# Optimization experiments

Measured on AMD Instinct MI355X. Metric: run time of the kernel, lower is better.

## Reference

```python
import jax, jax.numpy as jnp
import numpy as np

D_MODEL = 1024
N_HEADS = 16
D_K = D_MODEL // N_HEADS
THETA = 10000.0
NEG_INF = -1e30


def _rope_tables(token_positions, d_k, theta=THETA):
    # freqs[t, i] = t / theta**(2i/d_k), i in [0, d_k/2)
    exponent = jnp.arange(0, d_k, 2, dtype=jnp.float32)  # [d_k/2]
    inv_freq = 1.0 / theta ** (exponent / d_k)
    freqs = token_positions.astype(jnp.float32)[:, None] * inv_freq[None, :]  # [s, d_k/2]
    return jnp.cos(freqs), jnp.sin(freqs)


def _apply_rope(x, cos, sin):
    # x: [..., s, d_k]; interleaved pair rotation (pairs are (x[2i], x[2i+1]))
    x1 = x[..., 0::2]
    x2 = x[..., 1::2]
    r1 = x1 * cos - x2 * sin
    r2 = x1 * sin + x2 * cos
    return jnp.stack([r1, r2], axis=-1).reshape(x.shape)


def setup_inputs() -> dict:
    key = jax.random.key(0)
    ks = jax.random.split(key, 5)
    b, s = 2, 2048
    scale = np.sqrt(2.0 / (D_MODEL + D_MODEL))
    return {
        "x": jax.random.normal(ks[0], (b, s, D_MODEL), dtype=jnp.float32),
        "Wq": jax.random.normal(ks[1], (D_MODEL, D_MODEL), dtype=jnp.float32) * scale,
        "Wk": jax.random.normal(ks[2], (D_MODEL, D_MODEL), dtype=jnp.float32) * scale,
        "Wv": jax.random.normal(ks[3], (D_MODEL, D_MODEL), dtype=jnp.float32) * scale,
        "Wo": jax.random.normal(ks[4], (D_MODEL, D_MODEL), dtype=jnp.float32) * scale,
        "token_positions": jnp.arange(s, dtype=jnp.int64 if jax.config.jax_enable_x64 else jnp.int32),
    }


def reference(x, Wq, Wk, Wv, Wo, token_positions):
    b, s, _ = x.shape
    # QKV projections: weight stored [in, out]
    q = jnp.einsum('bsi,io->bso', x, Wq)
    k = jnp.einsum('bsi,io->bso', x, Wk)
    v = jnp.einsum('bsi,io->bso', x, Wv)
    # split heads: [b, h, s, d_k]
    q = q.reshape(b, s, N_HEADS, D_K).transpose(0, 2, 1, 3)
    k = k.reshape(b, s, N_HEADS, D_K).transpose(0, 2, 1, 3)
    v = v.reshape(b, s, N_HEADS, D_K).transpose(0, 2, 1, 3)
    # RoPE
    cos, sin = _rope_tables(token_positions, D_K)
    q = _apply_rope(q, cos, sin)
    k = _apply_rope(k, cos, sin)
    # causal attention with full materialized scores (faithful to source)
    scores = jnp.einsum('bhid,bhjd->bhij', q, k) / jnp.sqrt(jnp.float32(D_K))
    mask = jnp.tril(jnp.ones((s, s), dtype=bool))
    scores = jnp.where(mask, scores, NEG_INF)
    probs = jax.nn.softmax(scores, axis=-1)
    out = jnp.einsum('bhij,bhjd->bhid', probs, v)
    out = out.transpose(0, 2, 1, 3).reshape(b, s, D_MODEL)
    return jnp.einsum('bsi,io->bso', out, Wo)
```

## Files before the change

kernel.cpp:

```cpp
#include <hip/hip_runtime.h>
#include <hip/hip_bf16.h>
#include <cmath>

#define S_LEN 2048
#define DMODEL 1024
#define NHEADS 16
#define DK 64
#define BATCH 2
#define MTOT (BATCH * S_LEN)

using short8 = __attribute__((ext_vector_type(8))) short;
using floatx4 = __attribute__((ext_vector_type(4))) float;

__device__ __forceinline__ unsigned short f2b(float f) {
    union { float f; unsigned u; } v; v.f = f;
    unsigned r = v.u + 0x7fff + ((v.u >> 16) & 1);
    return (unsigned short)(r >> 16);
}

__device__ __forceinline__ unsigned pack2(float a, float b) {
    float2 t; t.x = a; t.y = b;
    __hip_bfloat162 h = __float22bfloat162_rn(t);
    union { __hip_bfloat162 h; unsigned u; } v; v.h = h;
    return v.u;
}

__device__ __forceinline__ void gload16(const void* g, void* l) {
    __builtin_amdgcn_global_load_lds(
        (const __attribute__((address_space(1))) unsigned int*)g,
        (__attribute__((address_space(3))) unsigned int*)l, 16, 0, 0);
}

#define FENCE() asm volatile("" ::: "memory")

__global__ __launch_bounds__(256) void prep_k(
    const float* __restrict__ x, unsigned short* __restrict__ xb,
    const int* __restrict__ tokpos, float* __restrict__ ct, float* __restrict__ st,
    const float* W0, const float* W1, const float* W2, const float* W3,
    unsigned short* T0, unsigned short* T1, unsigned short* T2, unsigned short* T3) {
    __shared__ float t[64][65];
    const int b = blockIdx.x;
    if (b < 2048) {
        int i = (b * 256 + threadIdx.x) * 8;
        float4 a = *(const float4*)(x + i);
        float4 bb = *(const float4*)(x + i + 4);
        short8 o;
        o[0] = f2b(a.x); o[1] = f2b(a.y); o[2] = f2b(a.z); o[3] = f2b(a.w);
        o[4] = f2b(bb.x); o[5] = f2b(bb.y); o[6] = f2b(bb.z); o[7] = f2b(bb.w);
        *(short8*)(xb + i) = o;
    } else if (b < 2304) {
        int idx = (b - 2048) * 256 + threadIdx.x;
        int si = idx >> 5;
        int ip = idx & 31;
        float pos = (float)tokpos[si];
        float inv_freq = powf(10000.0f, -(float)(2 * ip) / 64.0f);
        float ang = pos * inv_freq;
        ct[idx] = cosf(ang);
        st[idx] = sinf(ang);
    } else {
        int id = b - 2304;
        int z = id >> 8;
        int bx = id & 15, by = (id >> 4) & 15;
        const float* W = z == 0 ? W0 : z == 1 ? W1 : z == 2 ? W2 : W3;
        unsigned short* T = z == 0 ? T0 : z == 1 ? T1 : z == 2 ? T2 : T3;
        const bool perm = (z < 2);
        int n0 = bx * 64, k0 = by * 64;
        int rr = threadIdx.x >> 6, cc = threadIdx.x & 63;
#pragma unroll
        for (int r = 0; r < 16; r++) {
            int row = r * 4 + rr;
            t[row][cc] = W[(size_t)(k0 + row) * DMODEL + n0 + cc];
        }
        __syncthreads();
#pragma unroll
        for (int r = 0; r < 16; r++) {
            int row = r * 4 + rr;
            int drow = perm ? (((row & 1) ? 32 : 0) + (row >> 1)) : row;
            T[(size_t)(n0 + drow) * DMODEL + k0 + cc] = f2b(t[cc][row]);
        }
    }
}

__global__ __launch_bounds__(256) void add_k(float* __restrict__ out,
                                             const float* __restrict__ p) {
    int i = (blockIdx.x * 256 + threadIdx.x) * 8;
    float4 a = *(const float4*)(out + i);
    float4 b = *(const float4*)(p + i);
    float4 c = *(const float4*)(out + i + 4);
    float4 d = *(const float4*)(p + i + 4);
    a.x += b.x; a.y += b.y; a.z += b.z; a.w += b.w;
    c.x += d.x; c.y += d.y; c.z += d.z; c.w += d.w;
    *(float4*)(out + i) = a;
    *(float4*)(out + i + 4) = c;
}

__global__ __launch_bounds__(256) void vtrans_k(const unsigned short* __restrict__ V,
                                                unsigned short* __restrict__ Vt) {
    __shared__ unsigned short t[64][72];
    const int tid = threadIdx.x;
    const int s0 = blockIdx.x * 64, d0 = blockIdx.y * 64;
    const int bb = s0 >> 11;
#pragma unroll
    for (int it = 0; it < 4; it++) {
        int e = (it * 256 + tid) * 4;
        int r = e >> 6, c = e & 63;
        *(ushort4*)&t[r][c] = *(const ushort4*)(V + (size_t)(s0 + r) * DMODEL + d0 + c);
    }
    __syncthreads();
#pragma unroll
    for (int it = 0; it < 4; it++) {
        int e = (it * 256 + tid) * 4;
        int r = e >> 6, c = e & 63;
        ushort4 v;
        v.x = t[c + 0][r]; v.y = t[c + 1][r];
        v.z = t[c + 2][r]; v.w = t[c + 3][r];
        *(ushort4*)(Vt + (size_t)(bb * 1024 + d0 + r) * S_LEN + (s0 & (S_LEN - 1)) + c) = v;
    }
}

__global__ __launch_bounds__(512, 2) void mm_k(
    const unsigned short* __restrict__ A,
    const unsigned short* __restrict__ Bt0, const unsigned short* __restrict__ Bt1,
    const unsigned short* __restrict__ Bt2,
    void* C0, void* C1, void* C2,
    const float* __restrict__ ct, const float* __restrict__ st, int kind) {
    __shared__ __align__(16) unsigned short blob[10 * 8192];

    const int z = blockIdx.z;
    const unsigned short* Bt = (kind == 1) ? Bt0 : (z == 0 ? Bt0 : z == 1 ? Bt1 : Bt2);
    void* C = (kind == 1) ? (z == 0 ? C0 : C1) : (z == 0 ? C0 : z == 1 ? C1 : C2);
    const int mode = (kind == 1) ? 0 : (z == 2 ? 3 : 1);
    const int t0 = (kind == 1) ? z * 8 : 0;
    const int NT = (kind == 1) ? 8 : 16;
    const float qscale = (z == 0 && kind == 0) ? 0.18033688011112042f : 1.0f;

    const int tid = threadIdx.x;
    const int w = tid >> 6, lane = tid & 63;
    const int l15 = lane & 15, quad = lane >> 4;
    const int wr = w >> 2, wc = w & 3;
    const int m0 = blockIdx.x * 256, n0 = blockIdx.y * 256;

    const int rbase = (w >> 1) * 16 + l15;
    const int cbase = (w & 1) * 32 + quad * 8;

    floatx4 acc[8][4];
#pragma unroll
    for (int i = 0; i < 8; i++)
#pragma unroll
        for (int j = 0; j < 4; j++) acc[i][j] = (floatx4){0.f, 0.f, 0.f, 0.f};

    auto stage_half = [&](int h) {
        const int ts = t0 + (h >> 2), part = h & 3;
        const int slot = h % 10;
        const unsigned short* src =
            (part < 2 ? A + (((size_t)(m0 + part * 128 + rbase)) << 10)
                      : Bt + (((size_t)(n0 + (part - 2) * 128 + rbase)) << 10))
            + (size_t)ts * 64 + cbase;
        char* d = (char*)blob + slot * 16384 + w * 1024;
        gload16(src, d);
        gload16(src + (64 << 10), d + 8192);
    };

#pragma unroll
    for (int h = 0; h < 6; ++h) stage_half(h);
    asm volatile("s_waitcnt vmcnt(4)" ::: "memory");
    FENCE(); __builtin_amdgcn_s_barrier(); FENCE();

    short8 af[4][2];
    for (int t = 0; t < NT; ++t) {
        const int sb = (4 * t) % 10;
        int sA = sb + wr;            if (sA >= 10) sA -= 10;
        int sB = sb + 2 + (wc >> 1); if (sB >= 10) sB -= 10;
        const char* LA = (const char*)blob + sA * 16384;
        const char* LB = (const char*)blob + sB * 16384;
#pragma unroll
        for (int q = 0; q < 4; ++q) {
            const int rh = q >> 1, ch = q & 1;
            if (ch == 0) {
#pragma unroll
                for (int ii = 0; ii < 4; ++ii)
#pragma unroll
                    for (int kh = 0; kh < 2; ++kh)
                        af[ii][kh] = *(const short8*)(LA + ((rh * 4 + ii) * 2 + kh) * 1024 + lane * 16);
            }
            short8 bf[2][2];
#pragma unroll
            for (int jj = 0; jj < 2; ++jj)
#pragma unroll
                for (int kh = 0; kh < 2; ++kh)
                    bf[jj][kh] = *(const short8*)(LB + (((wc & 1) * 4 + ch * 2 + jj) * 2 + kh) * 1024 + lane * 16);
            const int h = 4 * t + q + 6;
            if (h < 4 * NT) stage_half(h);
            if (q == 3) {
                if (t == NT - 2) asm volatile("s_waitcnt vmcnt(0)" ::: "memory");
                else             asm volatile("s_waitcnt vmcnt(4)" ::: "memory");
            }
            FENCE(); __builtin_amdgcn_s_barrier(); FENCE();
            __builtin_amdgcn_s_setprio(1);
#pragma unroll
            for (int ii = 0; ii < 4; ++ii)
#pragma unroll
                for (int jj = 0; jj < 2; ++jj) {
                    floatx4 a0 = acc[rh * 4 + ii][ch * 2 + jj];
                    a0 = __builtin_amdgcn_mfma_f32_16x16x32_bf16(af[ii][0], bf[jj][0], a0, 0, 0, 0);
                    a0 = __builtin_amdgcn_mfma_f32_16x16x32_bf16(af[ii][1], bf[jj][1], a0, 0, 0, 0);
                    acc[rh * 4 + ii][ch * 2 + jj] = a0;
                }
            __builtin_amdgcn_s_setprio(0);
            FENCE(); __builtin_amdgcn_s_barrier(); FENCE();
        }
    }

#pragma unroll
    for (int i = 0; i < 8; i++) {
        const int rowb = m0 + wr * 128 + i * 16 + quad * 4;
        if (mode == 0) {
            float* Cf = (float*)C;
#pragma unroll
            for (int j = 0; j < 4; j++) {
                int colb = n0 + wc * 64 + j * 16 + l15;
#pragma unroll
                for (int r = 0; r < 4; r++)
                    Cf[(size_t)(rowb + r) * DMODEL + colb] = acc[i][j][r];
            }
        } else if (mode == 1) {
            unsigned short* Cb = (unsigned short*)C;
#pragma unroll
            for (int jh = 0; jh < 2; jh++) {
                int ip = jh * 16 + l15;
                int cole = n0 + wc * 64 + jh * 16 + l15;
#pragma unroll
                for (int r = 0; r < 4; r++) {
                    int row = rowb + r;
                    int si = row & (S_LEN - 1);
                    float c = ct[si * 32 + ip] * qscale;
                    float s = st[si * 32 + ip] * qscale;
                    float e = acc[i][jh][r];
                    float od = acc[i][jh + 2][r];
                    Cb[(size_t)row * DMODEL + cole] = f2b(e * c - od * s);
                    Cb[(size_t)row * DMODEL + cole + 32] = f2b(e * s + od * c);
                }
            }
        } else {
            unsigned short* Cb = (unsigned short*)C;
#pragma unroll
            for (int j = 0; j < 4; j++) {
                int colb = n0 + wc * 64 + j * 16 + l15;
#pragma unroll
                for (int r = 0; r < 4; r++)
                    Cb[(size_t)(rowb + r) * DMODEL + colb] = f2b(acc[i][j][r]);
            }
        }
    }
}

__global__ __launch_bounds__(512) void attn_k(const unsigned short* __restrict__ Q,
                                              const unsigned short* __restrict__ K,
                                              const unsigned short* __restrict__ Vt,
                                              unsigned short* __restrict__ O) {
    __shared__ __align__(16) unsigned short Kblob[2][4096];
    __shared__ __align__(16) unsigned short Vblob[2][4096];
    __shared__ __align__(16) unsigned short Ps[8][16 * 72];

    const int tid = threadIdx.x;
    const int w = tid >> 6, lane = tid & 63;
    const int l15 = lane & 15, quad = lane >> 4;
    const int idx = blockIdx.x;
    const int qt = 15 - (idx >> 5);
    const int bh = idx & 31;
    const int bb = bh >> 4, h = bh & 15;
    const int qbase = qt * 128 + w * 16;
    const int qrow = qbase + l15;

    const size_t qoff = (size_t)(bb * S_LEN + qbase + l15) * DMODEL + h * DK;
    short8 aq0 = *(const short8*)(Q + qoff + quad * 8);
    short8 aq1 = *(const short8*)(Q + qoff + 32 + quad * 8);

    floatx4 o[4];
#pragma unroll
    for (int f = 0; f < 4; f++) o[f] = (floatx4){0.f, 0.f, 0.f, 0.f};
    float mv = -1e30f, lv = 0.f;

    const unsigned short* Kb = K + (size_t)(bb * S_LEN) * DMODEL + h * DK;
    const unsigned short* Vb = Vt + (size_t)(bb * 1024 + h * DK) * S_LEN;
    unsigned short* ps = &Ps[w][0];

    auto stage = [&](int b, int kb) {
#pragma unroll
        for (int it = 0; it < 2; it++) {
            int g = it * 8 + w;
            if (g < 8) {
                const unsigned short* gp =
                    Kb + (size_t)(kb + (g >> 1) * 16 + l15) * DMODEL + (g & 1) * 32 + quad * 8;
                gload16(gp, (char*)&Kblob[b][0] + g * 1024);
            } else {
                int gv = g - 8;
                const unsigned short* gp =
                    Vb + (size_t)((gv >> 1) * 16 + l15) * S_LEN + kb + (gv & 1) * 32 + quad * 8;
                gload16(gp, (char*)&Vblob[b][0] + gv * 1024);
            }
        }
    };

    const int nkt = 2 * qt + 2;
    stage(0, 0);
    for (int kt = 0; kt < nkt; kt++) {
        const int b = kt & 1;
        const int kb = kt * 64;
        __syncthreads();
        if (kt + 1 < nkt) stage(b ^ 1, (kt + 1) * 64);

        if (kb <= qbase + 15) {
            const unsigned short* kbb = &Kblob[b][0];
            floatx4 c[4];
            __builtin_amdgcn_s_setprio(1);
#pragma unroll
            for (int g = 0; g < 4; g++) {
                short8 kf0 = *(const short8*)(kbb + (g * 2 + 0) * 512 + lane * 8);
                short8 kf1 = *(const short8*)(kbb + (g * 2 + 1) * 512 + lane * 8);
                floatx4 t = {0.f, 0.f, 0.f, 0.f};
                t = __builtin_amdgcn_mfma_f32_16x16x32_bf16(kf0, aq0, t, 0, 0, 0);
                c[g] = __builtin_amdgcn_mfma_f32_16x16x32_bf16(kf1, aq1, t, 0, 0, 0);
            }
            __builtin_amdgcn_s_setprio(0);

            float sv[16];
            if (kb + 63 <= qbase) {
#pragma unroll
                for (int g = 0; g < 4; g++)
#pragma unroll
                    for (int r = 0; r < 4; r++) sv[g * 4 + r] = c[g][r];
            } else {
#pragma unroll
                for (int g = 0; g < 4; g++)
#pragma unroll
                    for (int r = 0; r < 4; r++) {
                        int key = kb + g * 16 + quad * 4 + r;
                        sv[g * 4 + r] = (key <= qrow) ? c[g][r] : -1e30f;
                    }
            }
            float t0 = fmaxf(fmaxf(sv[0], sv[1]), sv[2]);
            float t1 = fmaxf(fmaxf(sv[3], sv[4]), sv[5]);
            float t2 = fmaxf(fmaxf(sv[6], sv[7]), sv[8]);
            float t3 = fmaxf(fmaxf(sv[9], sv[10]), sv[11]);
            float t4 = fmaxf(fmaxf(sv[12], sv[13]), sv[14]);
            float mx = fmaxf(fmaxf(fmaxf(t0, t1), fmaxf(t2, t3)), fmaxf(t4, sv[15]));
            mx = fmaxf(mx, __shfl_xor(mx, 16));
            mx = fmaxf(mx, __shfl_xor(mx, 32));

            if (!__all(mx <= mv)) {
                float mnew = fmaxf(mv, mx);
                float alpha = exp2f(mv - mnew);
                mv = mnew;
                lv *= alpha;
#pragma unroll
                for (int f = 0; f < 4; f++) {
                    o[f][0] *= alpha; o[f][1] *= alpha;
                    o[f][2] *= alpha; o[f][3] *= alpha;
                }
            }
            float p[16], psum = 0.f;
#pragma unroll
            for (int i = 0; i < 16; i++) {
                p[i] = exp2f(sv[i] - mv);
                psum += p[i];
            }
            lv += psum;

#pragma unroll
            for (int g = 0; g < 4; g++) {
                uint2 pk;
                pk.x = pack2(p[g * 4 + 0], p[g * 4 + 1]);
                pk.y = pack2(p[g * 4 + 2], p[g * 4 + 3]);
                *(uint2*)(ps + l15 * 72 + g * 16 + quad * 4) = pk;
            }
            short8 pf0 = *(const short8*)(ps + l15 * 72 + quad * 8);
            short8 pf1 = *(const short8*)(ps + l15 * 72 + 32 + quad * 8);
            const unsigned short* vbb = &Vblob[b][0];
            __builtin_amdgcn_s_setprio(1);
#pragma unroll
            for (int f = 0; f < 4; f++) {
                short8 vf0 = *(const short8*)(vbb + (f * 2 + 0) * 512 + lane * 8);
                short8 vf1 = *(const short8*)(vbb + (f * 2 + 1) * 512 + lane * 8);
                o[f] = __builtin_amdgcn_mfma_f32_16x16x32_bf16(vf0, pf0, o[f], 0, 0, 0);
                o[f] = __builtin_amdgcn_mfma_f32_16x16x32_bf16(vf1, pf1, o[f], 0, 0, 0);
            }
            __builtin_amdgcn_s_setprio(0);
        }
    }

    lv += __shfl_xor(lv, 16);
    lv += __shfl_xor(lv, 32);
    float inv = 1.0f / lv;
    __syncthreads();
#pragma unroll
    for (int f = 0; f < 4; f++) {
        uint2 pk;
        pk.x = pack2(o[f][0] * inv, o[f][1] * inv);
        pk.y = pack2(o[f][2] * inv, o[f][3] * inv);
        *(uint2*)(ps + l15 * 72 + f * 16 + quad * 4) = pk;
    }
    short8 r0 = *(const short8*)(ps + l15 * 72 + quad * 8);
    short8 r1 = *(const short8*)(ps + l15 * 72 + 32 + quad * 8);
    size_t obase = (size_t)(bb * S_LEN + qbase + l15) * DMODEL + h * DK;
    *(short8*)(O + obase + quad * 8) = r0;
    *(short8*)(O + obase + 32 + quad * 8) = r1;
}

extern "C" void kernel_launch(void* const* d_in, const int* in_sizes, int n_in,
                              void* d_out, int out_size, void* d_ws,
                              size_t ws_size, hipStream_t stream) {
    const float* x = (const float*)d_in[0];
    const float* Wq = (const float*)d_in[1];
    const float* Wk = (const float*)d_in[2];
    const float* Wv = (const float*)d_in[3];
    const float* Wo = (const float*)d_in[4];
    const int* tokpos = (const int*)d_in[5];
    float* out = (float*)d_out;

    const size_t MD = (size_t)MTOT * DMODEL;
    const size_t WD = (size_t)DMODEL * DMODEL;
    unsigned short* xb = (unsigned short*)d_ws;
    unsigned short* Wqt = xb + MD;
    unsigned short* Wkt = Wqt + WD;
    unsigned short* Wvt = Wkt + WD;
    unsigned short* Wot = Wvt + WD;
    unsigned short* Q = Wot + WD;
    unsigned short* K = Q + MD;
    unsigned short* V = K + MD;
    unsigned short* Vt = V + MD;
    float* ct = (float*)(Vt + MD);
    float* st = ct + S_LEN * 32;
    unsigned short* O = V;
    float* P1 = (float*)Q;

    prep_k<<<dim3(3328), dim3(256), 0, stream>>>(x, xb, tokpos, ct, st,
                                                 Wq, Wk, Wv, Wo, Wqt, Wkt, Wvt, Wot);

    mm_k<<<dim3(16, 4, 3), dim3(512), 0, stream>>>(xb, Wqt, Wkt, Wvt,
                                                   (void*)Q, (void*)K, (void*)V, ct, st, 0);
    vtrans_k<<<dim3(64, 16), dim3(256), 0, stream>>>(V, Vt);
    attn_k<<<dim3(512), dim3(512), 0, stream>>>(Q, K, Vt, O);
    mm_k<<<dim3(16, 4, 2), dim3(512), 0, stream>>>(O, Wot, Wot, Wot,
                                                   (void*)out, (void*)P1, (void*)P1, ct, st, 1);
    add_k<<<dim3(2048), dim3(256), 0, stream>>>(out, P1);
}
```

Baseline: 211.2 us.

## Process two 16-row query groups per wave in attention, halving block width

The attention kernel now runs 4 waves per block instead of 8, and each wave handles 32 query rows as two 16-row groups. Each K and V fragment read from shared memory feeds MFMAs for both groups, which halves LDS reads per unit of compute, and each wave carries two independent MFMA chains. The cost is roughly double the accumulator and softmax register state per wave and fewer waves per block, which may cut occupancy and the latency hiding that came from having more waves. The causal skip is now decided per 32-row band, so some MFMA work on fully masked tiles is added.

```diff
diff --git a/kernel.cpp b/kernel.cpp
--- a/kernel.cpp
+++ b/kernel.cpp
@@ -254,13 +254,13 @@
     }
 }
 
-__global__ __launch_bounds__(512) void attn_k(const unsigned short* __restrict__ Q,
+__global__ __launch_bounds__(256) void attn_k(const unsigned short* __restrict__ Q,
                                               const unsigned short* __restrict__ K,
                                               const unsigned short* __restrict__ Vt,
                                               unsigned short* __restrict__ O) {
     __shared__ __align__(16) unsigned short Kblob[2][4096];
     __shared__ __align__(16) unsigned short Vblob[2][4096];
-    __shared__ __align__(16) unsigned short Ps[8][16 * 72];
+    __shared__ __align__(16) unsigned short Ps[4][32 * 72];
 
     const int tid = threadIdx.x;
     const int w = tid >> 6, lane = tid & 63;
@@ -269,17 +269,22 @@
     const int qt = 15 - (idx >> 5);
     const int bh = idx & 31;
     const int bb = bh >> 4, h = bh & 15;
-    const int qbase = qt * 128 + w * 16;
-    const int qrow = qbase + l15;
-
-    const size_t qoff = (size_t)(bb * S_LEN + qbase + l15) * DMODEL + h * DK;
-    short8 aq0 = *(const short8*)(Q + qoff + quad * 8);
-    short8 aq1 = *(const short8*)(Q + qoff + 32 + quad * 8);
-
-    floatx4 o[4];
-#pragma unroll
-    for (int f = 0; f < 4; f++) o[f] = (floatx4){0.f, 0.f, 0.f, 0.f};
-    float mv = -1e30f, lv = 0.f;
+    const int qb_w = qt * 128 + w * 32;
+
+    short8 aq[2][2];
+#pragma unroll
+    for (int qg = 0; qg < 2; qg++) {
+        const size_t qoff = (size_t)(bb * S_LEN + qb_w + qg * 16 + l15) * DMODEL + h * DK;
+        aq[qg][0] = *(const short8*)(Q + qoff + quad * 8);
+        aq[qg][1] = *(const short8*)(Q + qoff + 32 + quad * 8);
+    }
+
+    floatx4 o[2][4];
+#pragma unroll
+    for (int qg = 0; qg < 2; qg++)
+#pragma unroll
+        for (int f = 0; f < 4; f++) o[qg][f] = (floatx4){0.f, 0.f, 0.f, 0.f};
+    float mv[2] = {-1e30f, -1e30f}, lv[2] = {0.f, 0.f};
 
     const unsigned short* Kb = K + (size_t)(bb * S_LEN) * DMODEL + h * DK;
     const unsigned short* Vb = Vt + (size_t)(bb * 1024 + h * DK) * S_LEN;
@@ -287,8 +292,8 @@
 
     auto stage = [&](int b, int kb) {
 #pragma unroll
-        for (int it = 0; it < 2; it++) {
-            int g = it * 8 + w;
+        for (int it = 0; it < 4; it++) {
+            int g = it * 4 + w;
             if (g < 8) {
                 const unsigned short* gp =
                     Kb + (size_t)(kb + (g >> 1) * 16 + l15) * DMODEL + (g & 1) * 32 + quad * 8;
@@ -310,101 +315,119 @@
         __syncthreads();
         if (kt + 1 < nkt) stage(b ^ 1, (kt + 1) * 64);
 
-        if (kb <= qbase + 15) {
+        if (kb <= qb_w + 31) {
             const unsigned short* kbb = &Kblob[b][0];
-            floatx4 c[4];
+            floatx4 c[4][2];
             __builtin_amdgcn_s_setprio(1);
 #pragma unroll
             for (int g = 0; g < 4; g++) {
                 short8 kf0 = *(const short8*)(kbb + (g * 2 + 0) * 512 + lane * 8);
                 short8 kf1 = *(const short8*)(kbb + (g * 2 + 1) * 512 + lane * 8);
-                floatx4 t = {0.f, 0.f, 0.f, 0.f};
-                t = __builtin_amdgcn_mfma_f32_16x16x32_bf16(kf0, aq0, t, 0, 0, 0);
-                c[g] = __builtin_amdgcn_mfma_f32_16x16x32_bf16(kf1, aq1, t, 0, 0, 0);
+#pragma unroll
+                for (int qg = 0; qg < 2; qg++) {
+                    floatx4 t = {0.f, 0.f, 0.f, 0.f};
+                    t = __builtin_amdgcn_mfma_f32_16x16x32_bf16(kf0, aq[qg][0], t, 0, 0, 0);
+                    c[g][qg] = __builtin_amdgcn_mfma_f32_16x16x32_bf16(kf1, aq[qg][1], t, 0, 0, 0);
+                }
             }
             __builtin_amdgcn_s_setprio(0);
 
-            float sv[16];
-            if (kb + 63 <= qbase) {
-#pragma unroll
-                for (int g = 0; g < 4; g++)
-#pragma unroll
-                    for (int r = 0; r < 4; r++) sv[g * 4 + r] = c[g][r];
-            } else {
-#pragma unroll
-                for (int g = 0; g < 4; g++)
-#pragma unroll
-                    for (int r = 0; r < 4; r++) {
-                        int key = kb + g * 16 + quad * 4 + r;
-                        sv[g * 4 + r] = (key <= qrow) ? c[g][r] : -1e30f;
+#pragma unroll
+            for (int qg = 0; qg < 2; qg++) {
+                const int qbg = qb_w + qg * 16;
+                const int qrow = qbg + l15;
+                float sv[16];
+                if (kb + 63 <= qbg) {
+#pragma unroll
+                    for (int g = 0; g < 4; g++)
+#pragma unroll
+                        for (int r = 0; r < 4; r++) sv[g * 4 + r] = c[g][qg][r];
+                } else {
+#pragma unroll
+                    for (int g = 0; g < 4; g++)
+#pragma unroll
+                        for (int r = 0; r < 4; r++) {
+                            int key = kb + g * 16 + quad * 4 + r;
+                            sv[g * 4 + r] = (key <= qrow) ? c[g][qg][r] : -1e30f;
+                        }
+                }
+                float t0 = fmaxf(fmaxf(sv[0], sv[1]), sv[2]);
+                float t1 = fmaxf(fmaxf(sv[3], sv[4]), sv[5]);
+                float t2 = fmaxf(fmaxf(sv[6], sv[7]), sv[8]);
+                float t3 = fmaxf(fmaxf(sv[9], sv[10]), sv[11]);
+                float t4 = fmaxf(fmaxf(sv[12], sv[13]), sv[14]);
+                float mx = fmaxf(fmaxf(fmaxf(t0, t1), fmaxf(t2, t3)), fmaxf(t4, sv[15]));
+                mx = fmaxf(mx, __shfl_xor(mx, 16));
+                mx = fmaxf(mx, __shfl_xor(mx, 32));
+
+                if (!__all(mx <= mv[qg])) {
+                    float mnew = fmaxf(mv[qg], mx);
+                    float alpha = exp2f(mv[qg] - mnew);
+                    mv[qg] = mnew;
+                    lv[qg] *= alpha;
+#pragma unroll
+                    for (int f = 0; f < 4; f++) {
+                        o[qg][f][0] *= alpha; o[qg][f][1] *= alpha;
+                        o[qg][f][2] *= alpha; o[qg][f][3] *= alpha;
                     }
-            }
-            float t0 = fmaxf(fmaxf(sv[0], sv[1]), sv[2]);
-            float t1 = fmaxf(fmaxf(sv[3], sv[4]), sv[5]);
-            float t2 = fmaxf(fmaxf(sv[6], sv[7]), sv[8]);
-            float t3 = fmaxf(fmaxf(sv[9], sv[10]), sv[11]);
-            float t4 = fmaxf(fmaxf(sv[12], sv[13]), sv[14]);
-            float mx = fmaxf(fmaxf(fmaxf(t0, t1), fmaxf(t2, t3)), fmaxf(t4, sv[15]));
-            mx = fmaxf(mx, __shfl_xor(mx, 16));
-            mx = fmaxf(mx, __shfl_xor(mx, 32));
-
-            if (!__all(mx <= mv)) {
-                float mnew = fmaxf(mv, mx);
-                float alpha = exp2f(mv - mnew);
-                mv = mnew;
-                lv *= alpha;
-#pragma unroll
-                for (int f = 0; f < 4; f++) {
-                    o[f][0] *= alpha; o[f][1] *= alpha;
-                    o[f][2] *= alpha; o[f][3] *= alpha;
-                }
-            }
-            float p[16], psum = 0.f;
-#pragma unroll
-            for (int i = 0; i < 16; i++) {
-                p[i] = exp2f(sv[i] - mv);
-                psum += p[i];
-            }
-            lv += psum;
-
-#pragma unroll
-            for (int g = 0; g < 4; g++) {
-                uint2 pk;
-                pk.x = pack2(p[g * 4 + 0], p[g * 4 + 1]);
-                pk.y = pack2(p[g * 4 + 2], p[g * 4 + 3]);
-                *(uint2*)(ps + l15 * 72 + g * 16 + quad * 4) = pk;
-            }
-            short8 pf0 = *(const short8*)(ps + l15 * 72 + quad * 8);
-            short8 pf1 = *(const short8*)(ps + l15 * 72 + 32 + quad * 8);
+                }
+                float p[16], psum = 0.f;
+#pragma unroll
+                for (int i = 0; i < 16; i++) {
+                    p[i] = exp2f(sv[i] - mv[qg]);
+                    psum += p[i];
+                }
+                lv[qg] += psum;
+
+#pragma unroll
+                for (int g = 0; g < 4; g++) {
+                    uint2 pk;
+                    pk.x = pack2(p[g * 4 + 0], p[g * 4 + 1]);
+                    pk.y = pack2(p[g * 4 + 2], p[g * 4 + 3]);
+                    *(uint2*)(ps + (qg * 16 + l15) * 72 + g * 16 + quad * 4) = pk;
+                }
+            }
+
+            short8 pf[2][2];
+#pragma unroll
+            for (int qg = 0; qg < 2; qg++) {
+                pf[qg][0] = *(const short8*)(ps + (qg * 16 + l15) * 72 + quad * 8);
+                pf[qg][1] = *(const short8*)(ps + (qg * 16 + l15) * 72 + 32 + quad * 8);
+            }
             const unsigned short* vbb = &Vblob[b][0];
             __builtin_amdgcn_s_setprio(1);
 #pragma unroll
             for (int f = 0; f < 4; f++) {
                 short8 vf0 = *(const short8*)(vbb + (f * 2 + 0) * 512 + lane * 8);
                 short8 vf1 = *(const short8*)(vbb + (f * 2 + 1) * 512 + lane * 8);
-                o[f] = __builtin_amdgcn_mfma_f32_16x16x32_bf16(vf0, pf0, o[f], 0, 0, 0);
-                o[f] = __builtin_amdgcn_mfma_f32_16x16x32_bf16(vf1, pf1, o[f], 0, 0, 0);
+#pragma unroll
+                for (int qg = 0; qg < 2; qg++) {
+                    o[qg][f] = __builtin_amdgcn_mfma_f32_16x16x32_bf16(vf0, pf[qg][0], o[qg][f], 0, 0, 0);
+                    o[qg][f] = __builtin_amdgcn_mfma_f32_16x16x32_bf16(vf1, pf[qg][1], o[qg][f], 0, 0, 0);
+                }
             }
             __builtin_amdgcn_s_setprio(0);
         }
     }
 
-    lv += __shfl_xor(lv, 16);
-    lv += __shfl_xor(lv, 32);
-    float inv = 1.0f / lv;
-    __syncthreads();
-#pragma unroll
-    for (int f = 0; f < 4; f++) {
-        uint2 pk;
-        pk.x = pack2(o[f][0] * inv, o[f][1] * inv);
-        pk.y = pack2(o[f][2] * inv, o[f][3] * inv);
-        *(uint2*)(ps + l15 * 72 + f * 16 + quad * 4) = pk;
-    }
-    short8 r0 = *(const short8*)(ps + l15 * 72 + quad * 8);
-    short8 r1 = *(const short8*)(ps + l15 * 72 + 32 + quad * 8);
-    size_t obase = (size_t)(bb * S_LEN + qbase + l15) * DMODEL + h * DK;
-    *(short8*)(O + obase + quad * 8) = r0;
-    *(short8*)(O + obase + 32 + quad * 8) = r1;
+#pragma unroll
+    for (int qg = 0; qg < 2; qg++) {
+        lv[qg] += __shfl_xor(lv[qg], 16);
+        lv[qg] += __shfl_xor(lv[qg], 32);
+        float inv = 1.0f / lv[qg];
+#pragma unroll
+        for (int f = 0; f < 4; f++) {
+            uint2 pk;
+            pk.x = pack2(o[qg][f][0] * inv, o[qg][f][1] * inv);
+            pk.y = pack2(o[qg][f][2] * inv, o[qg][f][3] * inv);
+            *(uint2*)(ps + (qg * 16 + l15) * 72 + f * 16 + quad * 4) = pk;
+        }
+        short8 r0 = *(const short8*)(ps + (qg * 16 + l15) * 72 + quad * 8);
+        short8 r1 = *(const short8*)(ps + (qg * 16 + l15) * 72 + 32 + quad * 8);
+        size_t obase = (size_t)(bb * S_LEN + qb_w + qg * 16 + l15) * DMODEL + h * DK;
+        *(short8*)(O + obase + quad * 8) = r0;
+        *(short8*)(O + obase + 32 + quad * 8) = r1;
+    }
 }
 
 extern "C" void kernel_launch(void* const* d_in, const int* in_sizes, int n_in,
@@ -440,7 +463,7 @@
     mm_k<<<dim3(16, 4, 3), dim3(512), 0, stream>>>(xb, Wqt, Wkt, Wvt,
                                                    (void*)Q, (void*)K, (void*)V, ct, st, 0);
     vtrans_k<<<dim3(64, 16), dim3(256), 0, stream>>>(V, Vt);
-    attn_k<<<dim3(512), dim3(512), 0, stream>>>(Q, K, Vt, O);
+    attn_k<<<dim3(512), dim3(256), 0, stream>>>(Q, K, Vt, O);
     mm_k<<<dim3(16, 4, 2), dim3(512), 0, stream>>>(O, Wot, Wot, Wot,
                                                    (void*)out, (void*)P1, (void*)P1, ct, st, 1);
     add_k<<<dim3(2048), dim3(256), 0, stream>>>(out, P1);
```

Measured after the change: 230.2 us. 9.0% more time.

## Split long causal attention query tiles across two blocks and merge partials

Applied to the files above, without the earlier changes.

The attention grid now uses a table-driven schedule where the six longest query tiles (qt 10-15) have their key range split into two halves, each processed by a separate block. Those blocks write unnormalized fp32 partial outputs plus running max and sum to scratch, and a new merge kernel combines them with log-sum-exp weighting and writes bf16 output. This targets load imbalance and the long tail of the causal triangle, and the schedule orders work roughly by size. The cost is an extra kernel launch, extra global traffic for fp32 partials, and scratch reuse of the xb buffer.

```diff
diff --git a/kernel.cpp b/kernel.cpp
--- a/kernel.cpp
+++ b/kernel.cpp
@@ -257,18 +257,30 @@
 __global__ __launch_bounds__(512) void attn_k(const unsigned short* __restrict__ Q,
                                               const unsigned short* __restrict__ K,
                                               const unsigned short* __restrict__ Vt,
-                                              unsigned short* __restrict__ O) {
+                                              unsigned short* __restrict__ O,
+                                              float* __restrict__ Ub,
+                                              float* __restrict__ MLb) {
     __shared__ __align__(16) unsigned short Kblob[2][4096];
     __shared__ __align__(16) unsigned short Vblob[2][4096];
     __shared__ __align__(16) unsigned short Ps[8][16 * 72];
+
+    static const int T_qt[22] = {9, 8, 15, 15, 7, 14, 14, 13, 13, 6, 12,
+                                 12, 11, 11, 5, 10, 10, 4, 3, 2, 1, 0};
+    static const int T_k0[22] = {0, 0, 0, 16, 0, 0, 15, 0, 14, 0, 0,
+                                 13, 0, 12, 0, 0, 11, 0, 0, 0, 0, 0};
+    static const int T_k1[22] = {20, 18, 16, 32, 16, 15, 30, 14, 28, 14, 13,
+                                 26, 12, 24, 12, 11, 22, 10, 8, 6, 4, 2};
+    static const int T_sx[22] = {-1, -1, 10, 11, -1, 8, 9, 6, 7, -1, 4,
+                                 5, 2, 3, -1, 0, 1, -1, -1, -1, -1, -1};
 
     const int tid = threadIdx.x;
     const int w = tid >> 6, lane = tid & 63;
     const int l15 = lane & 15, quad = lane >> 4;
     const int idx = blockIdx.x;
-    const int qt = 15 - (idx >> 5);
+    const int sr = idx >> 5;
     const int bh = idx & 31;
     const int bb = bh >> 4, h = bh & 15;
+    const int qt = T_qt[sr], kt0 = T_k0[sr], kt1 = T_k1[sr], sx = T_sx[sr];
     const int qbase = qt * 128 + w * 16;
     const int qrow = qbase + l15;
 
@@ -302,13 +314,12 @@
         }
     };
 
-    const int nkt = 2 * qt + 2;
-    stage(0, 0);
-    for (int kt = 0; kt < nkt; kt++) {
-        const int b = kt & 1;
+    stage(0, kt0 * 64);
+    for (int kt = kt0; kt < kt1; kt++) {
+        const int b = (kt - kt0) & 1;
         const int kb = kt * 64;
         __syncthreads();
-        if (kt + 1 < nkt) stage(b ^ 1, (kt + 1) * 64);
+        if (kt + 1 < kt1) stage(b ^ 1, (kt + 1) * 64);
 
         if (kb <= qbase + 15) {
             const unsigned short* kbb = &Kblob[b][0];
@@ -389,22 +400,77 @@
         }
     }
 
-    lv += __shfl_xor(lv, 16);
-    lv += __shfl_xor(lv, 32);
-    float inv = 1.0f / lv;
-    __syncthreads();
-#pragma unroll
-    for (int f = 0; f < 4; f++) {
-        uint2 pk;
-        pk.x = pack2(o[f][0] * inv, o[f][1] * inv);
-        pk.y = pack2(o[f][2] * inv, o[f][3] * inv);
-        *(uint2*)(ps + l15 * 72 + f * 16 + quad * 4) = pk;
-    }
-    short8 r0 = *(const short8*)(ps + l15 * 72 + quad * 8);
-    short8 r1 = *(const short8*)(ps + l15 * 72 + 32 + quad * 8);
-    size_t obase = (size_t)(bb * S_LEN + qbase + l15) * DMODEL + h * DK;
-    *(short8*)(O + obase + quad * 8) = r0;
-    *(short8*)(O + obase + 32 + quad * 8) = r1;
+    if (sx >= 0) {
+        const int slot = sx * 32 + bh;
+        float* up = Ub + (size_t)slot * 8192 + tid * 16;
+#pragma unroll
+        for (int f = 0; f < 4; f++) {
+            float4 v; v.x = o[f][0]; v.y = o[f][1]; v.z = o[f][2]; v.w = o[f][3];
+            *(float4*)(up + f * 4) = v;
+        }
+        float* mlp = MLb + (size_t)slot * 1024 + tid * 2;
+        mlp[0] = mv;
+        mlp[1] = lv;
+    } else {
+        lv += __shfl_xor(lv, 16);
+        lv += __shfl_xor(lv, 32);
+        float inv = 1.0f / lv;
+        __syncthreads();
+#pragma unroll
+        for (int f = 0; f < 4; f++) {
+            uint2 pk;
+            pk.x = pack2(o[f][0] * inv, o[f][1] * inv);
+            pk.y = pack2(o[f][2] * inv, o[f][3] * inv);
+            *(uint2*)(ps + l15 * 72 + f * 16 + quad * 4) = pk;
+        }
+        short8 r0 = *(const short8*)(ps + l15 * 72 + quad * 8);
+        short8 r1 = *(const short8*)(ps + l15 * 72 + 32 + quad * 8);
+        size_t obase = (size_t)(bb * S_LEN + qbase + l15) * DMODEL + h * DK;
+        *(short8*)(O + obase + quad * 8) = r0;
+        *(short8*)(O + obase + 32 + quad * 8) = r1;
+    }
+}
+
+__global__ __launch_bounds__(256) void mrg_k(const float* __restrict__ Ub,
+                                             const float* __restrict__ MLb,
+                                             unsigned short* __restrict__ O) {
+    const int pid = blockIdx.x;
+    const int qt = 10 + (pid >> 5);
+    const int bh = pid & 31;
+    const int bb = bh >> 4, h = bh & 15;
+    const int slotA = ((qt - 10) * 2) * 32 + bh;
+    const int slotB = slotA + 32;
+    const int tid = threadIdx.x;
+    const int q = tid >> 1, dh = tid & 1;
+    const int tq = (q >> 4) * 64 + (q & 15);
+
+    const float* mlA = MLb + (size_t)slotA * 1024;
+    const float* mlB = MLb + (size_t)slotB * 1024;
+    float mA = mlA[tq * 2], mB = mlB[tq * 2];
+    float lA = 0.f, lB = 0.f;
+#pragma unroll
+    for (int qd = 0; qd < 4; qd++) {
+        lA += mlA[(tq + qd * 16) * 2 + 1];
+        lB += mlB[(tq + qd * 16) * 2 + 1];
+    }
+    float m = fmaxf(mA, mB);
+    float wA = exp2f(mA - m), wB = exp2f(mB - m);
+    float inv = 1.0f / (lA * wA + lB * wB);
+
+    const float* uA = Ub + (size_t)slotA * 8192;
+    const float* uB = Ub + (size_t)slotB * 8192;
+    unsigned short ov[32];
+#pragma unroll
+    for (int dd = 0; dd < 32; dd++) {
+        int d = dh * 32 + dd;
+        int uoff = ((q >> 4) * 64 + ((d >> 2) & 3) * 16 + (q & 15)) * 16 + (d >> 4) * 4 + (d & 3);
+        float v = (uA[uoff] * wA + uB[uoff] * wB) * inv;
+        ov[dd] = f2b(v);
+    }
+    size_t obase = (size_t)(bb * S_LEN + qt * 128 + q) * DMODEL + h * DK + dh * 32;
+#pragma unroll
+    for (int c = 0; c < 4; c++)
+        *(short8*)(O + obase + c * 8) = *(short8*)&ov[c * 8];
 }
 
 extern "C" void kernel_launch(void* const* d_in, const int* in_sizes, int n_in,
@@ -433,6 +499,8 @@
     float* st = ct + S_LEN * 32;
     unsigned short* O = V;
     float* P1 = (float*)Q;
+    float* Ub = (float*)xb;
+    float* MLb = Ub + (size_t)384 * 8192;
 
     prep_k<<<dim3(3328), dim3(256), 0, stream>>>(x, xb, tokpos, ct, st,
                                                  Wq, Wk, Wv, Wo, Wqt, Wkt, Wvt, Wot);
@@ -440,7 +508,8 @@
     mm_k<<<dim3(16, 4, 3), dim3(512), 0, stream>>>(xb, Wqt, Wkt, Wvt,
                                                    (void*)Q, (void*)K, (void*)V, ct, st, 0);
     vtrans_k<<<dim3(64, 16), dim3(256), 0, stream>>>(V, Vt);
-    attn_k<<<dim3(512), dim3(512), 0, stream>>>(Q, K, Vt, O);
+    attn_k<<<dim3(704), dim3(512), 0, stream>>>(Q, K, Vt, O, Ub, MLb);
+    mrg_k<<<dim3(192), dim3(256), 0, stream>>>(Ub, MLb, O);
     mm_k<<<dim3(16, 4, 2), dim3(512), 0, stream>>>(O, Wot, Wot, Wot,
                                                    (void*)out, (void*)P1, (void*)P1, ct, st, 1);
     add_k<<<dim3(2048), dim3(256), 0, stream>>>(out, P1);
```

New measurement: 212.2 us. About the same (+0.5%).
